# Kernel optimization log

Hardware: AMD Instinct MI355X
Metric: run time of the kernel (lower is better)

## Reference

```python
import jax, jax.numpy as jnp
import numpy as np

D_MODEL = 512
N_HEADS = 8
HEAD_DIM = D_MODEL // N_HEADS
DEPTH = 6
N_LAYERS = 2 * DEPTH  # ['self','cross'] * depth
EPS_ATTN = 1e-6
EPS_LN = 1e-5


def _xavier(key, shape):
    fan_in, fan_out = shape[0], shape[1]
    a = jnp.sqrt(6.0 / (fan_in + fan_out))
    return jax.random.uniform(key, shape, jnp.float32, -a, a)


def setup_inputs() -> dict:
    key = jax.random.key(0)
    ks = jax.random.split(key, 10)
    N, L, C = 4, 4096, D_MODEL
    feat0 = jax.random.normal(ks[0], (N, L, C), jnp.float32)
    feat1 = jax.random.normal(ks[1], (N, L, C), jnp.float32)
    # stacked per-layer params; Linear stored as [in, out] so y = x @ W
    Wq = _xavier(ks[2], (C, C))[None].repeat(N_LAYERS, 0) * 0 + jnp.stack([_xavier(jax.random.fold_in(ks[2], i), (C, C)) for i in range(N_LAYERS)])
    Wk = jnp.stack([_xavier(jax.random.fold_in(ks[3], i), (C, C)) for i in range(N_LAYERS)])
    Wv = jnp.stack([_xavier(jax.random.fold_in(ks[4], i), (C, C)) for i in range(N_LAYERS)])
    Wm = jnp.stack([_xavier(jax.random.fold_in(ks[5], i), (C, C)) for i in range(N_LAYERS)])
    W1 = jnp.stack([_xavier(jax.random.fold_in(ks[6], i), (2 * C, 2 * C)) for i in range(N_LAYERS)])
    W2 = jnp.stack([_xavier(jax.random.fold_in(ks[7], i), (2 * C, C)) for i in range(N_LAYERS)])
    g1 = jnp.ones((N_LAYERS, C), jnp.float32)
    b1 = jnp.zeros((N_LAYERS, C), jnp.float32)
    g2 = jnp.ones((N_LAYERS, C), jnp.float32)
    b2 = jnp.zeros((N_LAYERS, C), jnp.float32)
    return dict(feat0=feat0, feat1=feat1, Wq=Wq, Wk=Wk, Wv=Wv, Wm=Wm,
                W1=W1, W2=W2, g1=g1, b1=b1, g2=g2, b2=b2)


def _layer_norm(x, g, b):
    mu = jnp.mean(x, -1, keepdims=True)
    var = jnp.mean(jnp.square(x - mu), -1, keepdims=True)
    return (x - mu) * jax.lax.rsqrt(var + EPS_LN) * g + b


def _encoder_layer(x, src, p):
    # x: [N,L,C], src: [N,S,C]
    Wq, Wk, Wv, Wm, W1, W2, g1, b1, g2, b2 = p
    N, L, C = x.shape
    S = src.shape[1]
    q = (x @ Wq).reshape(N, L, N_HEADS, HEAD_DIM)
    k = (src @ Wk).reshape(N, S, N_HEADS, HEAD_DIM)
    v = (src @ Wv).reshape(N, S, N_HEADS, HEAD_DIM)
    # linear attention: elu feature map, O(S*d^2)
    Q = jax.nn.elu(q) + 1.0
    K = jax.nn.elu(k) + 1.0
    v = v / S
    KV = jnp.einsum('nshd,nshv->nhdv', K, v)            # [N,H,D,D]
    Z = 1.0 / (jnp.einsum('nlhd,nhd->nlh', Q, K.sum(1)) + EPS_ATTN)
    msg = jnp.einsum('nlhd,nhdv,nlh->nlhv', Q, KV, Z) * S  # [N,L,H,D]
    msg = msg.reshape(N, L, C) @ Wm
    msg = _layer_norm(msg, g1, b1)
    msg = jnp.concatenate([x, msg], axis=-1)            # [N,L,2C]
    msg = jax.nn.relu(msg @ W1) @ W2
    msg = _layer_norm(msg, g2, b2)
    return x + msg


def reference(feat0, feat1, Wq, Wk, Wv, Wm, W1, W2, g1, b1, g2, b2):
    for i in range(N_LAYERS):
        p = (Wq[i], Wk[i], Wv[i], Wm[i], W1[i], W2[i], g1[i], b1[i], g2[i], b2[i])
        if i % 2 == 0:  # 'self'
            feat0 = _encoder_layer(feat0, feat0, p)
            feat1 = _encoder_layer(feat1, feat1, p)
        else:           # 'cross' (sequential: feat1 sees updated feat0)
            feat0 = _encoder_layer(feat0, feat1, p)
            feat1 = _encoder_layer(feat1, feat0, p)
    return feat0, feat1
```

## Files before the change

kernel.cpp:

```cpp
#include <hip/hip_runtime.h>

typedef __attribute__((ext_vector_type(8))) short short8;
typedef __attribute__((ext_vector_type(4))) float f32x4;
typedef __attribute__((ext_vector_type(8))) unsigned short ushort8;

__device__ inline float bf2f(unsigned short u) {
    unsigned int x = ((unsigned int)u) << 16;
    float f; __builtin_memcpy(&f, &x, 4); return f;
}
__device__ inline unsigned short f2bf(float f) {
    unsigned int x; __builtin_memcpy(&x, &f, 4);
    x += 0x7fffu + ((x >> 16) & 1u);
    return (unsigned short)(x >> 16);
}
__device__ inline float readf(const void* p, size_t i, int flag) {
    if (flag == 1) return bf2f(((const unsigned short*)p)[i]);
    if (flag == 2) return (float)(((const _Float16*)p)[i]);
    return ((const float*)p)[i];
}

__device__ __forceinline__ void gld_lds16(const unsigned short* g, unsigned short* l) {
    __builtin_amdgcn_global_load_lds(
        (const __attribute__((address_space(1))) unsigned int*)g,
        (__attribute__((address_space(3))) unsigned int*)l, 16, 0, 0);
}

__global__ void detect_dtype(const unsigned int* g1, int* flag) {
    unsigned int w = g1[0];
    int f = 0;
    if ((w & 0xFFFFu) == 0x3F80u) f = 1;
    else if ((w & 0xFFFFu) == 0x3C00u) f = 2;
    *flag = f;
}

__global__ void transpose_in(const void* __restrict__ in, unsigned short* __restrict__ out,
                             int R, int Cc, size_t inBS, int layer0, size_t outLS,
                             const int* flagp) {
    int flag = *flagp;
    int layer = layer0 + blockIdx.z;
    unsigned short* op = out + (size_t)blockIdx.z * outLS;
    __shared__ unsigned short tile[32][33];
    int c0 = blockIdx.x * 32, r0 = blockIdx.y * 32;
#pragma unroll
    for (int j = 0; j < 4; j++) {
        int r = r0 + threadIdx.y + j * 8;
        size_t src = (size_t)layer * inBS + (size_t)r * Cc + c0 + threadIdx.x;
        tile[threadIdx.y + j * 8][threadIdx.x] = f2bf(readf(in, src, flag));
    }
    __syncthreads();
#pragma unroll
    for (int j = 0; j < 4; j++) {
        int c = c0 + threadIdx.y + j * 8;
        op[(size_t)c * R + r0 + threadIdx.x] = tile[threadIdx.x][threadIdx.y + j * 8];
    }
}

__global__ void cvt_feat(const void* __restrict__ in, float* __restrict__ f32,
                         unsigned short* __restrict__ fbf, int n, const int* flagp) {
    int flag = *flagp;
    int i = blockIdx.x * 256 + threadIdx.x;
    if (i < n) {
        float v = readf(in, i, flag);
        f32[i] = v;
        fbf[i] = f2bf(v);
    }
}

__global__ __launch_bounds__(256) void gemm_bf16(
    const unsigned short* __restrict__ A, const unsigned short* __restrict__ A2,
    const unsigned short* __restrict__ BT, unsigned short* __restrict__ C,
    int M, int N, int K, int lda, int splitK, int ldb, int relu) {
    __shared__ __align__(16) unsigned short As[128 * 32];
    __shared__ __align__(16) unsigned short Bs[128 * 32];
    int t = threadIdx.x;
    int rowBase = blockIdx.y * 128, colBase = blockIdx.x * 128;
    int lane = t & 63, wave = t >> 6;
    int wm = (wave & 1) * 64, wn = (wave >> 1) * 64;
    int mrow = lane & 15, quad = lane >> 4;
    f32x4 acc[4][4];
#pragma unroll
    for (int i = 0; i < 4; i++)
#pragma unroll
        for (int j = 0; j < 4; j++) acc[i][j] = (f32x4){0.f, 0.f, 0.f, 0.f};

    int r0 = t >> 2, c0 = (t & 3) * 8;
    int r1 = r0 + 64;

    for (int k0 = 0; k0 < K; k0 += 32) {
        const unsigned short* Ab; int kk;
        if (k0 < splitK) { Ab = A; kk = k0; } else { Ab = A2; kk = k0 - splitK; }
        __syncthreads();
        gld_lds16(Ab + (size_t)(rowBase + r0) * lda + kk + c0, &As[t * 8]);
        gld_lds16(Ab + (size_t)(rowBase + r1) * lda + kk + c0, &As[2048 + t * 8]);
        gld_lds16(BT + (size_t)(colBase + r0) * ldb + k0 + c0, &Bs[t * 8]);
        gld_lds16(BT + (size_t)(colBase + r1) * ldb + k0 + c0, &Bs[2048 + t * 8]);
        __syncthreads();
        short8 af[4], bfr[4];
#pragma unroll
        for (int mt = 0; mt < 4; mt++)
            af[mt] = *reinterpret_cast<const short8*>(&As[(wm + mt * 16 + mrow) * 32 + quad * 8]);
#pragma unroll
        for (int nt = 0; nt < 4; nt++)
            bfr[nt] = *reinterpret_cast<const short8*>(&Bs[(wn + nt * 16 + mrow) * 32 + quad * 8]);
#pragma unroll
        for (int mt = 0; mt < 4; mt++)
#pragma unroll
            for (int nt = 0; nt < 4; nt++)
                acc[mt][nt] = __builtin_amdgcn_mfma_f32_16x16x32_bf16(af[mt], bfr[nt], acc[mt][nt], 0, 0, 0);
    }
#pragma unroll
    for (int mt = 0; mt < 4; mt++)
#pragma unroll
        for (int nt = 0; nt < 4; nt++)
#pragma unroll
            for (int r = 0; r < 4; r++) {
                int row = rowBase + wm + mt * 16 + quad * 4 + r;
                int col = colBase + wn + nt * 16 + mrow;
                float v = acc[mt][nt][r];
                if (relu) v = fmaxf(v, 0.f);
                C[(size_t)row * N + col] = f2bf(v);
            }
}

__global__ __launch_bounds__(256) void kv_reduce(
    const unsigned short* __restrict__ kv, float* __restrict__ KV, float* __restrict__ Ksum) {
    __shared__ float smem[4096];
    float* kf = smem;
    float* vf = smem + 2048;
    int t = threadIdx.x;
    int sc = blockIdx.x, h = blockIdx.y, n = blockIdx.z;
    int w = t >> 6, u = t & 63;
    int d0 = (u >> 3) * 8, e0 = (u & 7) * 8;
    float acc[8][8];
#pragma unroll
    for (int i = 0; i < 8; i++)
#pragma unroll
        for (int j = 0; j < 8; j++) acc[i][j] = 0.f;
    float ks[8];
#pragma unroll
    for (int i = 0; i < 8; i++) ks[i] = 0.f;

    int rl = t >> 3, dg = (t & 7) << 3;
    for (int sb = 0; sb < 8; sb++) {
        int srow = n * 4096 + sc * 256 + sb * 32 + rl;
        const unsigned short* kp = kv + (size_t)srow * 1024 + h * 64 + dg;
        ushort8 kr = *reinterpret_cast<const ushort8*>(kp);
        ushort8 vr = *reinterpret_cast<const ushort8*>(kp + 512);
        __syncthreads();
#pragma unroll
        for (int j = 0; j < 8; j++) {
            float x = bf2f(kr[j]);
            kf[rl * 64 + dg + j] = x > 0.f ? x + 1.f : __expf(x);
            vf[rl * 64 + dg + j] = bf2f(vr[j]);
        }
        __syncthreads();
#pragma unroll
        for (int r = 0; r < 8; r++) {
            int s = w * 8 + r;
            float4 ka = *reinterpret_cast<const float4*>(&kf[s * 64 + d0]);
            float4 kb = *reinterpret_cast<const float4*>(&kf[s * 64 + d0 + 4]);
            float4 va = *reinterpret_cast<const float4*>(&vf[s * 64 + e0]);
            float4 vb = *reinterpret_cast<const float4*>(&vf[s * 64 + e0 + 4]);
            float kreg[8] = {ka.x, ka.y, ka.z, ka.w, kb.x, kb.y, kb.z, kb.w};
            float vreg[8] = {va.x, va.y, va.z, va.w, vb.x, vb.y, vb.z, vb.w};
#pragma unroll
            for (int i = 0; i < 8; i++) ks[i] += kreg[i];
#pragma unroll
            for (int i = 0; i < 8; i++)
#pragma unroll
                for (int j = 0; j < 8; j++) acc[i][j] += kreg[i] * vreg[j];
        }
    }
    __syncthreads();
    if (w == 0) {
#pragma unroll
        for (int i = 0; i < 8; i++)
#pragma unroll
            for (int j = 0; j < 8; j++) smem[(d0 + i) * 64 + e0 + j] = acc[i][j];
    }
    __syncthreads();
#pragma unroll
    for (int ww = 1; ww < 4; ww++) {
        if (w == ww) {
#pragma unroll
            for (int i = 0; i < 8; i++)
#pragma unroll
                for (int j = 0; j < 8; j++) smem[(d0 + i) * 64 + e0 + j] += acc[i][j];
        }
        __syncthreads();
    }
    float* dst = KV + ((size_t)(n * 8 + h) << 12);
#pragma unroll
    for (int i = 0; i < 16; i++) {
        int idx = t + i * 256;
        atomicAdd(dst + idx, smem[idx]);
    }
    if ((u & 7) == 0) {
#pragma unroll
        for (int i = 0; i < 8; i++)
            atomicAdd(Ksum + (n * 8 + h) * 64 + d0 + i, ks[i]);
    }
}

__global__ __launch_bounds__(256) void attn_msg(
    const unsigned short* __restrict__ q, const float* __restrict__ KV,
    const float* __restrict__ Ksum, unsigned short* __restrict__ msg) {
    __shared__ __align__(16) float qsh[4][128];
    int t = threadIdx.x;
    int rcb = blockIdx.x, hp = blockIdx.y, n = blockIdx.z;
    int h0 = hp * 2;
    int w = t >> 6, lane = t & 63;

    const float* kvp = KV + (size_t)(n * 8 + h0) * 4096 + lane;
    float kv0[64], kv1[64];
#pragma unroll
    for (int d = 0; d < 64; d++) kv0[d] = kvp[d * 64];
#pragma unroll
    for (int d = 0; d < 64; d++) kv1[d] = kvp[4096 + d * 64];
    const float* ksp = Ksum + (size_t)(n * 8 + h0) * 64;
    float ks0 = ksp[lane * 2], ks1 = ksp[lane * 2 + 1];

    for (int it = 0; it < 32; it++) {
        int row = rcb * 128 + it * 4 + w;
        unsigned int raw = *reinterpret_cast<const unsigned int*>(
            q + (size_t)(n * 4096 + row) * 512 + h0 * 64 + lane * 2);
        float x0 = bf2f((unsigned short)(raw & 0xFFFFu));
        float x1 = bf2f((unsigned short)(raw >> 16));
        x0 = x0 > 0.f ? x0 + 1.f : __expf(x0);
        x1 = x1 > 0.f ? x1 + 1.f : __expf(x1);
        float part = x0 * ks0 + x1 * ks1;
#pragma unroll
        for (int off = 1; off < 32; off <<= 1) part += __shfl_xor(part, off, 64);
        float z0 = 1.f / (__shfl(part, 0, 64) + 1e-6f);
        float z1 = 1.f / (__shfl(part, 32, 64) + 1e-6f);
        qsh[w][lane * 2] = x0;
        qsh[w][lane * 2 + 1] = x1;
        float a0 = 0.f, a1 = 0.f;
#pragma unroll
        for (int d4 = 0; d4 < 16; d4++) {
            float4 qa = *reinterpret_cast<const float4*>(&qsh[w][d4 * 4]);
            float4 qb = *reinterpret_cast<const float4*>(&qsh[w][64 + d4 * 4]);
            a0 += qa.x * kv0[d4 * 4] + qa.y * kv0[d4 * 4 + 1] +
                  qa.z * kv0[d4 * 4 + 2] + qa.w * kv0[d4 * 4 + 3];
            a1 += qb.x * kv1[d4 * 4] + qb.y * kv1[d4 * 4 + 1] +
                  qb.z * kv1[d4 * 4 + 2] + qb.w * kv1[d4 * 4 + 3];
        }
        unsigned short* mp = msg + (size_t)(n * 4096 + row) * 512 + h0 * 64;
        mp[lane] = f2bf(a0 * z0);
        mp[64 + lane] = f2bf(a1 * z1);
    }
}

__global__ __launch_bounds__(256) void ln_fwd(
    const unsigned short* __restrict__ in, unsigned short* __restrict__ out,
    const void* __restrict__ g, const void* __restrict__ b, int layer, const int* flagp) {
    int flag = *flagp;
    int wave = threadIdx.x >> 6, lane = threadIdx.x & 63;
    size_t row = (size_t)blockIdx.x * 4 + wave;
    ushort8 raw = *reinterpret_cast<const ushort8*>(in + row * 512 + lane * 8);
    float x[8], s = 0.f, sq = 0.f;
#pragma unroll
    for (int j = 0; j < 8; j++) { x[j] = bf2f(raw[j]); s += x[j]; sq += x[j] * x[j]; }
#pragma unroll
    for (int off = 1; off < 64; off <<= 1) { s += __shfl_xor(s, off, 64); sq += __shfl_xor(sq, off, 64); }
    float mu = s * (1.f / 512.f);
    float var = fmaxf(sq * (1.f / 512.f) - mu * mu, 0.f);
    float rs = rsqrtf(var + 1e-5f);
    int c = layer * 512 + lane * 8;
    ushort8 o;
#pragma unroll
    for (int j = 0; j < 8; j++) {
        float gv = readf(g, c + j, flag);
        float bv = readf(b, c + j, flag);
        o[j] = f2bf((x[j] - mu) * rs * gv + bv);
    }
    *reinterpret_cast<ushort8*>(out + row * 512 + lane * 8) = o;
}

__global__ __launch_bounds__(256) void ln_res(
    const unsigned short* __restrict__ u, float* __restrict__ f32,
    unsigned short* __restrict__ fbf, const void* __restrict__ g,
    const void* __restrict__ b, int layer, const int* flagp) {
    int flag = *flagp;
    int wave = threadIdx.x >> 6, lane = threadIdx.x & 63;
    size_t row = (size_t)blockIdx.x * 4 + wave;
    ushort8 raw = *reinterpret_cast<const ushort8*>(u + row * 512 + lane * 8);
    float x[8], s = 0.f, sq = 0.f;
#pragma unroll
    for (int j = 0; j < 8; j++) { x[j] = bf2f(raw[j]); s += x[j]; sq += x[j] * x[j]; }
#pragma unroll
    for (int off = 1; off < 64; off <<= 1) { s += __shfl_xor(s, off, 64); sq += __shfl_xor(sq, off, 64); }
    float mu = s * (1.f / 512.f);
    float var = fmaxf(sq * (1.f / 512.f) - mu * mu, 0.f);
    float rs = rsqrtf(var + 1e-5f);
    int c = layer * 512 + lane * 8;
    float* fp = f32 + row * 512 + lane * 8;
    float4 f0 = *reinterpret_cast<float4*>(fp);
    float4 f1 = *reinterpret_cast<float4*>(fp + 4);
    float fv[8] = {f0.x, f0.y, f0.z, f0.w, f1.x, f1.y, f1.z, f1.w};
    ushort8 o;
#pragma unroll
    for (int j = 0; j < 8; j++) {
        float gv = readf(g, c + j, flag);
        float bv = readf(b, c + j, flag);
        float y = (x[j] - mu) * rs * gv + bv;
        fv[j] += y;
        o[j] = f2bf(fv[j]);
    }
    f0 = make_float4(fv[0], fv[1], fv[2], fv[3]);
    f1 = make_float4(fv[4], fv[5], fv[6], fv[7]);
    *reinterpret_cast<float4*>(fp) = f0;
    *reinterpret_cast<float4*>(fp + 4) = f1;
    *reinterpret_cast<ushort8*>(fbf + row * 512 + lane * 8) = o;
}

extern "C" void kernel_launch(void* const* d_in, const int* in_sizes, int n_in,
                              void* d_out, int out_size, void* d_ws, size_t ws_size,
                              hipStream_t stream) {
    char* ws = (char*)d_ws;
    size_t o = 0;
    auto take = [&](size_t bytes) { char* p = ws + o; o += (bytes + 1023) & ~(size_t)1023; return p; };
    unsigned short* wqTl  = (unsigned short*)take(262144ull * 2);
    unsigned short* wkvTl = (unsigned short*)take(524288ull * 2);
    unsigned short* wmTl  = (unsigned short*)take(262144ull * 2);
    unsigned short* w1Tl  = (unsigned short*)take(1048576ull * 2);
    unsigned short* w2Tl  = (unsigned short*)take(524288ull * 2);
    float* f32_0 = (float*)take(8388608ull * 4);
    float* f32_1 = (float*)take(8388608ull * 4);
    unsigned short* fbf0  = (unsigned short*)take(8388608ull * 2);
    unsigned short* fbf1  = (unsigned short*)take(8388608ull * 2);
    unsigned short* poolA = (unsigned short*)take(8388608ull * 2);
    unsigned short* poolB = (unsigned short*)take(16777216ull * 2);
    unsigned short* poolC = (unsigned short*)take(8388608ull * 2);
    float* kvws = (float*)take(133120ull * 4);
    int* flagp = (int*)take(64);
    float* ksumws = kvws + 131072;

    const size_t WPER = 2621440ull;
    bool preT = ws_size >= o + WPER * 12ull * 2ull + 65536ull;
    unsigned short* wAll = preT ? (unsigned short*)take(WPER * 12ull * 2ull) : nullptr;

    detect_dtype<<<1, 1, 0, stream>>>((const unsigned int*)d_in[8], flagp);
    cvt_feat<<<32768, 256, 0, stream>>>(d_in[0], f32_0, fbf0, 8388608, flagp);
    cvt_feat<<<32768, 256, 0, stream>>>(d_in[1], f32_1, fbf1, 8388608, flagp);

    if (preT) {
        transpose_in<<<dim3(16, 16, 12), dim3(32, 8), 0, stream>>>(d_in[2], wAll,           512, 512,  262144, 0, WPER, flagp);
        transpose_in<<<dim3(16, 16, 12), dim3(32, 8), 0, stream>>>(d_in[3], wAll + 262144,  512, 512,  262144, 0, WPER, flagp);
        transpose_in<<<dim3(16, 16, 12), dim3(32, 8), 0, stream>>>(d_in[4], wAll + 524288,  512, 512,  262144, 0, WPER, flagp);
        transpose_in<<<dim3(16, 16, 12), dim3(32, 8), 0, stream>>>(d_in[5], wAll + 786432,  512, 512,  262144, 0, WPER, flagp);
        transpose_in<<<dim3(32, 32, 12), dim3(32, 8), 0, stream>>>(d_in[6], wAll + 1048576, 1024, 1024, 1048576, 0, WPER, flagp);
        transpose_in<<<dim3(16, 32, 12), dim3(32, 8), 0, stream>>>(d_in[7], wAll + 2097152, 1024, 512,  524288, 0, WPER, flagp);
    }

    auto enc = [&](float* xf32, unsigned short* xbf, const unsigned short* srcbf, int l,
                   const unsigned short* wq_p, const unsigned short* wkv_p, const unsigned short* wm_p,
                   const unsigned short* w1_p, const unsigned short* w2_p) {
        gemm_bf16<<<dim3(4, 128), 256, 0, stream>>>(xbf, xbf, wq_p, poolA, 16384, 512, 512, 512, 512, 512, 0);
        gemm_bf16<<<dim3(8, 128), 256, 0, stream>>>(srcbf, srcbf, wkv_p, poolB, 16384, 1024, 512, 512, 512, 512, 0);
        hipMemsetAsync(kvws, 0, 133120ull * 4, stream);
        kv_reduce<<<dim3(16, 8, 4), 256, 0, stream>>>(poolB, kvws, ksumws);
        attn_msg<<<dim3(32, 4, 4), 256, 0, stream>>>(poolA, kvws, ksumws, poolC);
        gemm_bf16<<<dim3(4, 128), 256, 0, stream>>>(poolC, poolC, wm_p, poolA, 16384, 512, 512, 512, 512, 512, 0);
        ln_fwd<<<4096, 256, 0, stream>>>(poolA, poolC, d_in[8], d_in[9], l, flagp);
        gemm_bf16<<<dim3(8, 128), 256, 0, stream>>>(xbf, poolC, w1_p, poolB, 16384, 1024, 1024, 512, 512, 1024, 1);
        gemm_bf16<<<dim3(4, 128), 256, 0, stream>>>(poolB, poolB, w2_p, poolA, 16384, 512, 1024, 1024, 1024, 1024, 0);
        ln_res<<<4096, 256, 0, stream>>>(poolA, xf32, xbf, d_in[10], d_in[11], l, flagp);
    };

    for (int l = 0; l < 12; l++) {
        const unsigned short *wq_p, *wkv_p, *wm_p, *w1_p, *w2_p;
        if (preT) {
            unsigned short* base = wAll + (size_t)l * WPER;
            wq_p = base; wkv_p = base + 262144; wm_p = base + 786432;
            w1_p = base + 1048576; w2_p = base + 2097152;
        } else {
            transpose_in<<<dim3(16, 16), dim3(32, 8), 0, stream>>>(d_in[2], wqTl,            512, 512,  262144, l, 0, flagp);
            transpose_in<<<dim3(16, 16), dim3(32, 8), 0, stream>>>(d_in[3], wkvTl,           512, 512,  262144, l, 0, flagp);
            transpose_in<<<dim3(16, 16), dim3(32, 8), 0, stream>>>(d_in[4], wkvTl + 262144,  512, 512,  262144, l, 0, flagp);
            transpose_in<<<dim3(16, 16), dim3(32, 8), 0, stream>>>(d_in[5], wmTl,            512, 512,  262144, l, 0, flagp);
            transpose_in<<<dim3(32, 32), dim3(32, 8), 0, stream>>>(d_in[6], w1Tl,            1024, 1024, 1048576, l, 0, flagp);
            transpose_in<<<dim3(16, 32), dim3(32, 8), 0, stream>>>(d_in[7], w2Tl,            1024, 512,  524288, l, 0, flagp);
            wq_p = wqTl; wkv_p = wkvTl; wm_p = wmTl; w1_p = w1Tl; w2_p = w2Tl;
        }
        if ((l & 1) == 0) {
            enc(f32_0, fbf0, fbf0, l, wq_p, wkv_p, wm_p, w1_p, w2_p);
            enc(f32_1, fbf1, fbf1, l, wq_p, wkv_p, wm_p, w1_p, w2_p);
        } else {
            enc(f32_0, fbf0, fbf1, l, wq_p, wkv_p, wm_p, w1_p, w2_p);
            enc(f32_1, fbf1, fbf0, l, wq_p, wkv_p, wm_p, w1_p, w2_p);
        }
    }

    hipMemcpyAsync(d_out, f32_0, 8388608ull * 4, hipMemcpyDeviceToDevice, stream);
    hipMemcpyAsync((char*)d_out + 8388608ull * 4, f32_1, 8388608ull * 4, hipMemcpyDeviceToDevice, stream);
}
```

Baseline: 7.917 ms.

## Batch both feature streams in self layers and fuse QKV projection into one GEMM

For self-attention layers, when pre-transposed weights are available, both feature tensors are processed as a single batch of 8 sequences instead of two separate encoder passes. The Q, K and V projections run as one GEMM whose output columns are split between two buffers through a new column-split epilogue. The feature conversion kernel is also vectorised to handle 8 elements per thread. This halves the number of launches in self layers and gives each launch larger grids, at the cost of doubled scratch buffers. The batched path assumes fbf0/fbf1 and f32_0/f32_1 sit contiguously in the workspace and that the Wq, Wk and Wv transposes are laid out adjacently.

```diff
diff --git a/kernel.cpp b/kernel.cpp
--- a/kernel.cpp
+++ b/kernel.cpp
@@ -17,6 +17,9 @@
     if (flag == 1) return bf2f(((const unsigned short*)p)[i]);
     if (flag == 2) return (float)(((const _Float16*)p)[i]);
     return ((const float*)p)[i];
+}
+__device__ inline float h2f(unsigned short u) {
+    _Float16 h; __builtin_memcpy(&h, &u, 2); return (float)h;
 }
 
 __device__ __forceinline__ void gld_lds16(const unsigned short* g, unsigned short* l) {
@@ -58,18 +61,36 @@
 __global__ void cvt_feat(const void* __restrict__ in, float* __restrict__ f32,
                          unsigned short* __restrict__ fbf, int n, const int* flagp) {
     int flag = *flagp;
-    int i = blockIdx.x * 256 + threadIdx.x;
-    if (i < n) {
-        float v = readf(in, i, flag);
-        f32[i] = v;
-        fbf[i] = f2bf(v);
-    }
+    int i = (blockIdx.x * 256 + threadIdx.x) * 8;
+    if (i >= n) return;
+    float v[8];
+    if (flag == 1) {
+        ushort8 r = *reinterpret_cast<const ushort8*>((const unsigned short*)in + i);
+#pragma unroll
+        for (int j = 0; j < 8; j++) { unsigned short us = r[j]; v[j] = bf2f(us); }
+    } else if (flag == 2) {
+        ushort8 r = *reinterpret_cast<const ushort8*>((const unsigned short*)in + i);
+#pragma unroll
+        for (int j = 0; j < 8; j++) { unsigned short us = r[j]; v[j] = h2f(us); }
+    } else {
+        float4 a = *reinterpret_cast<const float4*>((const float*)in + i);
+        float4 b = *reinterpret_cast<const float4*>((const float*)in + i + 4);
+        v[0] = a.x; v[1] = a.y; v[2] = a.z; v[3] = a.w;
+        v[4] = b.x; v[5] = b.y; v[6] = b.z; v[7] = b.w;
+    }
+    *reinterpret_cast<float4*>(f32 + i) = make_float4(v[0], v[1], v[2], v[3]);
+    *reinterpret_cast<float4*>(f32 + i + 4) = make_float4(v[4], v[5], v[6], v[7]);
+    ushort8 o;
+#pragma unroll
+    for (int j = 0; j < 8; j++) o[j] = f2bf(v[j]);
+    *reinterpret_cast<ushort8*>(fbf + i) = o;
 }
 
 __global__ __launch_bounds__(256) void gemm_bf16(
     const unsigned short* __restrict__ A, const unsigned short* __restrict__ A2,
     const unsigned short* __restrict__ BT, unsigned short* __restrict__ C,
-    int M, int N, int K, int lda, int splitK, int ldb, int relu) {
+    unsigned short* __restrict__ C2,
+    int K, int lda, int splitK, int ldb, int ldc, int colSplit, int ldc2, int relu) {
     __shared__ __align__(16) unsigned short As[128 * 32];
     __shared__ __align__(16) unsigned short Bs[128 * 32];
     int t = threadIdx.x;
@@ -108,6 +129,9 @@
             for (int nt = 0; nt < 4; nt++)
                 acc[mt][nt] = __builtin_amdgcn_mfma_f32_16x16x32_bf16(af[mt], bfr[nt], acc[mt][nt], 0, 0, 0);
     }
+    unsigned short* Cout; int cb, ldco;
+    if (colBase < colSplit) { Cout = C; cb = colBase; ldco = ldc; }
+    else { Cout = C2; cb = colBase - colSplit; ldco = ldc2; }
 #pragma unroll
     for (int mt = 0; mt < 4; mt++)
 #pragma unroll
@@ -115,10 +139,10 @@
 #pragma unroll
             for (int r = 0; r < 4; r++) {
                 int row = rowBase + wm + mt * 16 + quad * 4 + r;
-                int col = colBase + wn + nt * 16 + mrow;
+                int col = cb + wn + nt * 16 + mrow;
                 float v = acc[mt][nt][r];
                 if (relu) v = fmaxf(v, 0.f);
-                C[(size_t)row * N + col] = f2bf(v);
+                Cout[(size_t)row * ldco + col] = f2bf(v);
             }
 }
 
@@ -149,9 +173,10 @@
         __syncthreads();
 #pragma unroll
         for (int j = 0; j < 8; j++) {
-            float x = bf2f(kr[j]);
+            unsigned short ku = kr[j], vu = vr[j];
+            float x = bf2f(ku);
             kf[rl * 64 + dg + j] = x > 0.f ? x + 1.f : __expf(x);
-            vf[rl * 64 + dg + j] = bf2f(vr[j]);
+            vf[rl * 64 + dg + j] = bf2f(vu);
         }
         __syncthreads();
 #pragma unroll
@@ -260,7 +285,7 @@
     ushort8 raw = *reinterpret_cast<const ushort8*>(in + row * 512 + lane * 8);
     float x[8], s = 0.f, sq = 0.f;
 #pragma unroll
-    for (int j = 0; j < 8; j++) { x[j] = bf2f(raw[j]); s += x[j]; sq += x[j] * x[j]; }
+    for (int j = 0; j < 8; j++) { unsigned short us = raw[j]; x[j] = bf2f(us); s += x[j]; sq += x[j] * x[j]; }
 #pragma unroll
     for (int off = 1; off < 64; off <<= 1) { s += __shfl_xor(s, off, 64); sq += __shfl_xor(sq, off, 64); }
     float mu = s * (1.f / 512.f);
@@ -287,7 +312,7 @@
     ushort8 raw = *reinterpret_cast<const ushort8*>(u + row * 512 + lane * 8);
     float x[8], s = 0.f, sq = 0.f;
 #pragma unroll
-    for (int j = 0; j < 8; j++) { x[j] = bf2f(raw[j]); s += x[j]; sq += x[j] * x[j]; }
+    for (int j = 0; j < 8; j++) { unsigned short us = raw[j]; x[j] = bf2f(us); s += x[j]; sq += x[j] * x[j]; }
 #pragma unroll
     for (int off = 1; off < 64; off <<= 1) { s += __shfl_xor(s, off, 64); sq += __shfl_xor(sq, off, 64); }
     float mu = s * (1.f / 512.f);
@@ -329,20 +354,20 @@
     float* f32_1 = (float*)take(8388608ull * 4);
     unsigned short* fbf0  = (unsigned short*)take(8388608ull * 2);
     unsigned short* fbf1  = (unsigned short*)take(8388608ull * 2);
-    unsigned short* poolA = (unsigned short*)take(8388608ull * 2);
-    unsigned short* poolB = (unsigned short*)take(16777216ull * 2);
-    unsigned short* poolC = (unsigned short*)take(8388608ull * 2);
-    float* kvws = (float*)take(133120ull * 4);
+    unsigned short* poolA = (unsigned short*)take(16777216ull * 2);
+    unsigned short* poolB = (unsigned short*)take(33554432ull * 2);
+    unsigned short* poolC = (unsigned short*)take(16777216ull * 2);
+    float* kvws = (float*)take(266240ull * 4);
     int* flagp = (int*)take(64);
-    float* ksumws = kvws + 131072;
+    float* ksumws = kvws + 262144;
 
     const size_t WPER = 2621440ull;
     bool preT = ws_size >= o + WPER * 12ull * 2ull + 65536ull;
     unsigned short* wAll = preT ? (unsigned short*)take(WPER * 12ull * 2ull) : nullptr;
 
     detect_dtype<<<1, 1, 0, stream>>>((const unsigned int*)d_in[8], flagp);
-    cvt_feat<<<32768, 256, 0, stream>>>(d_in[0], f32_0, fbf0, 8388608, flagp);
-    cvt_feat<<<32768, 256, 0, stream>>>(d_in[1], f32_1, fbf1, 8388608, flagp);
+    cvt_feat<<<4096, 256, 0, stream>>>(d_in[0], f32_0, fbf0, 8388608, flagp);
+    cvt_feat<<<4096, 256, 0, stream>>>(d_in[1], f32_1, fbf1, 8388608, flagp);
 
     if (preT) {
         transpose_in<<<dim3(16, 16, 12), dim3(32, 8), 0, stream>>>(d_in[2], wAll,           512, 512,  262144, 0, WPER, flagp);
@@ -353,19 +378,41 @@
         transpose_in<<<dim3(16, 32, 12), dim3(32, 8), 0, stream>>>(d_in[7], wAll + 2097152, 1024, 512,  524288, 0, WPER, flagp);
     }
 
-    auto enc = [&](float* xf32, unsigned short* xbf, const unsigned short* srcbf, int l,
-                   const unsigned short* wq_p, const unsigned short* wkv_p, const unsigned short* wm_p,
-                   const unsigned short* w1_p, const unsigned short* w2_p) {
-        gemm_bf16<<<dim3(4, 128), 256, 0, stream>>>(xbf, xbf, wq_p, poolA, 16384, 512, 512, 512, 512, 512, 0);
-        gemm_bf16<<<dim3(8, 128), 256, 0, stream>>>(srcbf, srcbf, wkv_p, poolB, 16384, 1024, 512, 512, 512, 512, 0);
-        hipMemsetAsync(kvws, 0, 133120ull * 4, stream);
+    auto enc1 = [&](float* xf32, unsigned short* xbf, const unsigned short* srcbf, int l,
+                    const unsigned short* wq_p, const unsigned short* wkv_p, const unsigned short* wm_p,
+                    const unsigned short* w1_p, const unsigned short* w2_p) {
+        gemm_bf16<<<dim3(4, 128), 256, 0, stream>>>(xbf, xbf, wq_p, poolA, poolA,
+            512, 512, 512, 512, 512, 512, 512, 0);
+        gemm_bf16<<<dim3(8, 128), 256, 0, stream>>>(srcbf, srcbf, wkv_p, poolB, poolB,
+            512, 512, 512, 512, 1024, 1024, 1024, 0);
+        (void)hipMemsetAsync(kvws, 0, 266240ull * 4, stream);
         kv_reduce<<<dim3(16, 8, 4), 256, 0, stream>>>(poolB, kvws, ksumws);
         attn_msg<<<dim3(32, 4, 4), 256, 0, stream>>>(poolA, kvws, ksumws, poolC);
-        gemm_bf16<<<dim3(4, 128), 256, 0, stream>>>(poolC, poolC, wm_p, poolA, 16384, 512, 512, 512, 512, 512, 0);
+        gemm_bf16<<<dim3(4, 128), 256, 0, stream>>>(poolC, poolC, wm_p, poolA, poolA,
+            512, 512, 512, 512, 512, 512, 512, 0);
         ln_fwd<<<4096, 256, 0, stream>>>(poolA, poolC, d_in[8], d_in[9], l, flagp);
-        gemm_bf16<<<dim3(8, 128), 256, 0, stream>>>(xbf, poolC, w1_p, poolB, 16384, 1024, 1024, 512, 512, 1024, 1);
-        gemm_bf16<<<dim3(4, 128), 256, 0, stream>>>(poolB, poolB, w2_p, poolA, 16384, 512, 1024, 1024, 1024, 1024, 0);
+        gemm_bf16<<<dim3(8, 128), 256, 0, stream>>>(xbf, poolC, w1_p, poolB, poolB,
+            1024, 512, 512, 1024, 1024, 1024, 1024, 1);
+        gemm_bf16<<<dim3(4, 128), 256, 0, stream>>>(poolB, poolB, w2_p, poolA, poolA,
+            1024, 1024, 1024, 1024, 512, 512, 512, 0);
         ln_res<<<4096, 256, 0, stream>>>(poolA, xf32, xbf, d_in[10], d_in[11], l, flagp);
+    };
+
+    auto enc2 = [&](int l, const unsigned short* wqkv_p, const unsigned short* wm_p,
+                    const unsigned short* w1_p, const unsigned short* w2_p) {
+        gemm_bf16<<<dim3(12, 256), 256, 0, stream>>>(fbf0, fbf0, wqkv_p, poolA, poolB,
+            512, 512, 512, 512, 512, 512, 1024, 0);
+        (void)hipMemsetAsync(kvws, 0, 266240ull * 4, stream);
+        kv_reduce<<<dim3(16, 8, 8), 256, 0, stream>>>(poolB, kvws, ksumws);
+        attn_msg<<<dim3(32, 4, 8), 256, 0, stream>>>(poolA, kvws, ksumws, poolC);
+        gemm_bf16<<<dim3(4, 256), 256, 0, stream>>>(poolC, poolC, wm_p, poolA, poolA,
+            512, 512, 512, 512, 512, 512, 512, 0);
+        ln_fwd<<<8192, 256, 0, stream>>>(poolA, poolC, d_in[8], d_in[9], l, flagp);
+        gemm_bf16<<<dim3(8, 256), 256, 0, stream>>>(fbf0, poolC, w1_p, poolB, poolB,
+            1024, 512, 512, 1024, 1024, 1024, 1024, 1);
+        gemm_bf16<<<dim3(4, 256), 256, 0, stream>>>(poolB, poolB, w2_p, poolA, poolA,
+            1024, 1024, 1024, 1024, 512, 512, 512, 0);
+        ln_res<<<8192, 256, 0, stream>>>(poolA, f32_0, fbf0, d_in[10], d_in[11], l, flagp);
     };
 
     for (int l = 0; l < 12; l++) {
@@ -384,14 +431,18 @@
             wq_p = wqTl; wkv_p = wkvTl; wm_p = wmTl; w1_p = w1Tl; w2_p = w2Tl;
         }
         if ((l & 1) == 0) {
-            enc(f32_0, fbf0, fbf0, l, wq_p, wkv_p, wm_p, w1_p, w2_p);
-            enc(f32_1, fbf1, fbf1, l, wq_p, wkv_p, wm_p, w1_p, w2_p);
+            if (preT) {
+                enc2(l, wq_p , wm_p, w1_p, w2_p);
+            } else {
+                enc1(f32_0, fbf0, fbf0, l, wq_p, wkv_p, wm_p, w1_p, w2_p);
+                enc1(f32_1, fbf1, fbf1, l, wq_p, wkv_p, wm_p, w1_p, w2_p);
+            }
         } else {
-            enc(f32_0, fbf0, fbf1, l, wq_p, wkv_p, wm_p, w1_p, w2_p);
-            enc(f32_1, fbf1, fbf0, l, wq_p, wkv_p, wm_p, w1_p, w2_p);
-        }
-    }
-
-    hipMemcpyAsync(d_out, f32_0, 8388608ull * 4, hipMemcpyDeviceToDevice, stream);
-    hipMemcpyAsync((char*)d_out + 8388608ull * 4, f32_1, 8388608ull * 4, hipMemcpyDeviceToDevice, stream);
-}
+            enc1(f32_0, fbf0, fbf1, l, wq_p, wkv_p, wm_p, w1_p, w2_p);
+            enc1(f32_1, fbf1, fbf0, l, wq_p, wkv_p, wm_p, w1_p, w2_p);
+        }
+    }
+
+    (void)hipMemcpyAsync(d_out, f32_0, 8388608ull * 4, hipMemcpyDeviceToDevice, stream);
+    (void)hipMemcpyAsync((char*)d_out + 8388608ull * 4, f32_1, 8388608ull * 4, hipMemcpyDeviceToDevice, stream);
+}
```

After: 8.228 ms. 3.9% more time.
